# Performance work log

Hardware: AMD Instinct MI355X
Metric: run time of the kernel (lower is better)

The kernel has to match this reference:

```python
import jax, jax.numpy as jnp
import numpy as np
from functools import partial

BANK = 256
ADDR = 64
OUT_C, IN_C, KH, KW = 64, 64, 3, 3
BS, H, W = 32, 128, 128


def setup_inputs() -> dict:
    key = jax.random.key(0)
    ks = jax.random.split(key, 6)
    x = jax.random.normal(ks[0], (BS, IN_C, H, W), dtype=jnp.float32)
    w_addr = jax.random.normal(ks[1], (BS, ADDR), dtype=jnp.float32)
    b_addr = jax.random.normal(ks[2], (BS, OUT_C, ADDR), dtype=jnp.float32)
    # learned parameters
    w_bank = jax.random.normal(ks[3], (BANK, OUT_C, IN_C, KH, KW), dtype=jnp.float32) * (1.0 / np.sqrt(IN_C * KH * KW))
    bound = 1.0 / np.sqrt(IN_C * KH * KW)
    b_bank = jax.random.uniform(ks[4], (BANK,), minval=-bound, maxval=bound, dtype=jnp.float32)
    address_space = jax.random.normal(ks[5], (BANK, ADDR), dtype=jnp.float32)
    return {"x": x, "w_addr": w_addr, "b_addr": b_addr, "w_bank": w_bank,
            "b_bank": b_bank, "address_space": address_space, "s": 1, "p": 1}


def _hyper_conv(x, w_addr, b_addr, w_bank, b_bank, address_space, s, p):
    # soft addressing: keys @ address_space.T -> softmax -> weighted sum of bank
    sel_w = jax.nn.softmax(w_addr @ address_space.T, axis=-1)          # [bs, bank]
    w = jnp.einsum('bn,noikl->boikl', sel_w, w_bank)                   # [bs, O, I, kh, kw]
    sel_b = jax.nn.softmax(b_addr @ address_space.T, axis=-1)          # [bs, O, bank]
    b = jnp.einsum('bon,n->bo', sel_b, b_bank)                         # [bs, O]

    def conv_one(xi, wi):
        # xi: [I, H, W], wi: [O, I, kh, kw]
        return jax.lax.conv_general_dilated(
            xi[None], wi, window_strides=(s, s), padding=[(p, p), (p, p)],
            dimension_numbers=('NCHW', 'OIHW', 'NCHW'))[0]

    o = jax.vmap(conv_one)(x, w)                                       # [bs, O, H', W']
    return o + b[:, :, None, None]


def reference(x, w_addr, b_addr, w_bank, b_bank, address_space, s, p):
    return _hyper_conv(x, w_addr, b_addr, w_bank, b_bank, address_space, int(s), int(p))
```

## Files before the change

### kernel.cpp

```cpp
#include <hip/hip_runtime.h>
#include <hip/hip_bf16.h>
#include <math.h>

#define BS   32
#define IC   64
#define OC   64
#define HH   128
#define WW   128
#define BANK 256
#define ADDR 64
#define WELEM (OC*IC*9)

#define XROW  (8 * 132 * 8)
#define XSAMP (130 * XROW)

typedef short short8 __attribute__((ext_vector_type(8)));
typedef float f32x16 __attribute__((ext_vector_type(16)));

__device__ __forceinline__ short f2bf(float f) {
    unsigned u = __builtin_bit_cast(unsigned, f);
    unsigned r = (u + 0x7FFFu + ((u >> 16) & 1u)) >> 16;
    return (short)r;
}

typedef __attribute__((address_space(3))) unsigned int lds_u32;
typedef const __attribute__((address_space(1))) unsigned int g_u32;
__device__ __forceinline__ void gload16(const short* g, short* l) {
    __builtin_amdgcn_global_load_lds((g_u32*)g, (lds_u32*)l, 16, 0, 0);
}

__global__ __launch_bounds__(BANK) void k_selw(const float* __restrict__ w_addr,
                                               const float* __restrict__ aspace,
                                               float* __restrict__ sel_w) {
    int b = blockIdx.x;
    int n = threadIdx.x;
    const float* wa = w_addr + b * ADDR;
    const float* as = aspace + n * ADDR;
    float dot = 0.f;
#pragma unroll
    for (int k = 0; k < ADDR; ++k) dot = fmaf(wa[k], as[k], dot);

    __shared__ float red[BANK];
    red[n] = dot; __syncthreads();
    for (int s = BANK / 2; s > 0; s >>= 1) {
        if (n < s) red[n] = fmaxf(red[n], red[n + s]);
        __syncthreads();
    }
    float m = red[0]; __syncthreads();
    float e = expf(dot - m);
    red[n] = e; __syncthreads();
    for (int s = BANK / 2; s > 0; s >>= 1) {
        if (n < s) red[n] += red[n + s];
        __syncthreads();
    }
    sel_w[b * BANK + n] = e / red[0];
}

__global__ __launch_bounds__(BANK) void k_bias(const float* __restrict__ b_addr,
                                               const float* __restrict__ aspace,
                                               const float* __restrict__ b_bank,
                                               float* __restrict__ bias) {
    int bo = blockIdx.x;
    int n  = threadIdx.x;
    const float* ba = b_addr + (size_t)bo * ADDR;
    const float* as = aspace + n * ADDR;
    float dot = 0.f;
#pragma unroll
    for (int k = 0; k < ADDR; ++k) dot = fmaf(ba[k], as[k], dot);

    __shared__ float red[BANK];
    red[n] = dot; __syncthreads();
    for (int s = BANK / 2; s > 0; s >>= 1) {
        if (n < s) red[n] = fmaxf(red[n], red[n + s]);
        __syncthreads();
    }
    float m = red[0]; __syncthreads();
    float e = expf(dot - m);
    red[n] = e; __syncthreads();
    for (int s = BANK / 2; s > 0; s >>= 1) {
        if (n < s) red[n] += red[n + s];
        __syncthreads();
    }
    float denom = red[0]; __syncthreads();
    red[n] = e * b_bank[n]; __syncthreads();
    for (int s = BANK / 2; s > 0; s >>= 1) {
        if (n < s) red[n] += red[n + s];
        __syncthreads();
    }
    if (n == 0) bias[bo] = red[0] / denom;
}

__global__ __launch_bounds__(256) void k_wmix(const float* __restrict__ sel_w,
                                              const float* __restrict__ w_bank,
                                              __hip_bfloat16* __restrict__ wmb) {
    __shared__ float s_red[4 * 32 * 64];

    int tid = threadIdx.x;
    int jl  = tid & 63;
    int c   = tid >> 6;
    int jb  = blockIdx.x * 64 + jl;

    int n0 = __builtin_amdgcn_readfirstlane(c * 64);
    const float* selp = sel_w + n0;

    float wv[64];
#pragma unroll
    for (int n = 0; n < 64; ++n)
        wv[n] = w_bank[(size_t)(n0 + n) * WELEM + jb];

    float acc[BS];
#pragma unroll
    for (int b = 0; b < BS; ++b) acc[b] = 0.f;
#pragma unroll
    for (int b = 0; b < BS; ++b)
#pragma unroll
        for (int n = 0; n < 64; ++n)
            acc[b] = fmaf(selp[b * BANK + n], wv[n], acc[b]);

#pragma unroll
    for (int b = 0; b < BS; ++b)
        s_red[(c * 32 + b) * 64 + jl] = acc[b];
    __syncthreads();

    int B0  = (tid * 8) & 31;
    int jl2 = (tid * 8) >> 5;
    int j   = blockIdx.x * 64 + jl2;
    int o   = j / 576;
    int rem = j - o * 576;
    int i   = rem / 9;
    int tap = rem - i * 9;
    size_t base = ((size_t)tap * 8 + (i >> 3)) * 512 + (size_t)o * 8 + (i & 7);
#pragma unroll
    for (int u = 0; u < 8; ++u) {
        int b = B0 + u;
        float v = s_red[(0 * 32 + b) * 64 + jl2] + s_red[(1 * 32 + b) * 64 + jl2]
                + s_red[(2 * 32 + b) * 64 + jl2] + s_red[(3 * 32 + b) * 64 + jl2];
        short sv = f2bf(v);
        wmb[(size_t)b * (9 * 8 * 64 * 8) + base] = *reinterpret_cast<__hip_bfloat16*>(&sv);
    }
}

__global__ __launch_bounds__(256) void k_tr(const float* __restrict__ x,
                                            short* __restrict__ xbf) {
    int bid = blockIdx.x;
    int b  = bid / 130;
    int ry = bid - b * 130;
    short* row = xbf + (size_t)b * XSAMP + (size_t)ry * XROW;
    int tid = threadIdx.x;
    short8 z = {0, 0, 0, 0, 0, 0, 0, 0};

    if (ry == 0 || ry == 129) {
        for (int u = tid; u < 1056; u += 256)
            *(short8*)(row + u * 8) = z;
        return;
    }
    int gy = ry - 1;
    const float* xb = x + ((size_t)b * IC * HH + gy) * WW;
    int icg = tid & 7;
    int px0 = (tid >> 3) * 4;

    float4 v[8];
#pragma unroll
    for (int e = 0; e < 8; ++e)
        v[e] = *(const float4*)&xb[(size_t)(icg * 8 + e) * HH * WW + px0];
#pragma unroll
    for (int p = 0; p < 4; ++p) {
        short8 s;
#pragma unroll
        for (int e = 0; e < 8; ++e)
            s[e] = f2bf(((const float*)&v[e])[p]);
        *(short8*)(row + ((size_t)icg * 132 + px0 + p + 1) * 8) = s;
    }
    if (tid < 32) {
        int g = tid >> 2;
        int sel = tid & 3;
        int cz = (sel == 0) ? 0 : (128 + sel);
        *(short8*)(row + ((size_t)g * 132 + cz) * 8) = z;
    }
}

__global__ __launch_bounds__(512) void k_conv(const short* __restrict__ xbf,
                                              const short* __restrict__ wmb,
                                              const float* __restrict__ bias,
                                              float* __restrict__ out) {
    __shared__ short s_x[2][8704];
    __shared__ short s_w[2][9216];
    __shared__ float s_bias[OC];

    int orig    = blockIdx.x;
    int logical = (orig & 7) * 256 + (orig >> 3);
    int b   = logical >> 6;
    int y0  = (logical & 63) * 2;
    int tid = threadIdx.x;
    int wv  = tid >> 6;
    int lane = tid & 63;
    int h   = lane >> 5;
    int ln  = lane & 31;
    int wr  = wv & 1;
    int oh  = (wv >> 1) & 1;
    int ph  = wv >> 2;

    if (tid < OC) s_bias[tid] = bias[b * OC + tid];

    const short* xs   = xbf + (size_t)b * XSAMP + (size_t)y0 * XROW;
    const short* wmbs = wmb + (size_t)b * 36864;

    auto stage = [&](int cc, int bf) {
        for (int i = wv; i < 17; i += 8) {
            int u  = i * 64 + lane;
            int uc = (u < 1056) ? u : 0;
            int ky  = uc / 264;
            int rem = uc - ky * 264;
            const short* g = xs + (size_t)ky * XROW + (size_t)(2 * cc * 132 + rem) * 8;
            gload16(g, &s_x[bf][i * 512]);
        }
        for (int j = wv; j < 18; j += 8) {
            int v   = j * 64 + lane;
            int tap = v >> 7;
            int wt  = v & 127;
            const short* g = wmbs + (size_t)((tap * 8 + 2 * cc) * 64 + wt) * 8;
            gload16(g, &s_w[bf][j * 512]);
        }
    };

    f32x16 acc[2];
    acc[0] = (f32x16)0.0f;
    acc[1] = (f32x16)0.0f;

    stage(0, 0);
    __syncthreads();

    for (int cc = 0; cc < 4; ++cc) {
        int bf = cc & 1;
        if (cc < 3) stage(cc + 1, bf ^ 1);
        const short8* xb8 = (const short8*)s_x[bf];
        const short8* wb8 = (const short8*)s_w[bf];
#pragma unroll
        for (int ky = 0; ky < 3; ++ky) {
#pragma unroll
            for (int kx = 0; kx < 3; ++kx) {
                short8 a = wb8[((ky * 3 + kx) * 2 + h) * 64 + oh * 32 + ln];
#pragma unroll
                for (int nt = 0; nt < 2; ++nt) {
                    short8 bb = xb8[((wr + ky) * 2 + h) * 132 + ph * 64 + nt * 32 + ln + kx];
                    acc[nt] = __builtin_amdgcn_mfma_f32_32x32x16_bf16(a, bb, acc[nt], 0, 0, 0);
                }
            }
        }
        __syncthreads();
    }

    int y = y0 + wr;
    float* ob = out + (size_t)b * OC * HH * WW;
#pragma unroll
    for (int nt = 0; nt < 2; ++nt) {
#pragma unroll
        for (int r = 0; r < 16; ++r) {
            int oc = oh * 32 + (r & 3) + 8 * (r >> 2) + 4 * h;
            int px = ph * 64 + nt * 32 + ln;
            ob[((size_t)oc * HH + y) * WW + px] = acc[nt][r] + s_bias[oc];
        }
    }
}

extern "C" void kernel_launch(void* const* d_in, const int* in_sizes, int n_in,
                              void* d_out, int out_size, void* d_ws, size_t ws_size,
                              hipStream_t stream) {
    const float* x      = (const float*)d_in[0];
    const float* w_addr = (const float*)d_in[1];
    const float* b_addr = (const float*)d_in[2];
    const float* w_bank = (const float*)d_in[3];
    const float* b_bank = (const float*)d_in[4];
    const float* aspace = (const float*)d_in[5];
    float* out = (float*)d_out;

    char* ws = (char*)d_ws;
    float*          sel_w = (float*)ws;
    float*          bias  = (float*)(ws + 32768);
    __hip_bfloat16* wmb   = (__hip_bfloat16*)(ws + 40960);
    short*          xbf   = (short*)(ws + 40960 + 2359296);

    k_selw<<<BS, BANK, 0, stream>>>(w_addr, aspace, sel_w);
    k_bias<<<BS * OC, BANK, 0, stream>>>(b_addr, aspace, b_bank, bias);
    k_wmix<<<WELEM / 64, 256, 0, stream>>>(sel_w, w_bank, wmb);
    k_tr<<<BS * 130, 256, 0, stream>>>(x, xbf);
    k_conv<<<BS * 64, 512, 0, stream>>>(xbf, (const short*)wmb, bias, out);
}
```

Before: 156.0 us.

## Fuse fp32-to-bf16 input transpose into conv kernel with register-staged prefetch

Removes the separate k_tr kernel and its padded bf16 scratch copy of x. The conv kernel now reads fp32 x directly, converts and packs it to bf16 on the fly, and writes it into LDS along with zeroed halo columns and zero rows at the borders. Loads for the next channel chunk go into registers before the MFMA loop and are stored to LDS after it, replacing the async global_load_lds copies. This saves one full read and write of x plus a launch. In exchange it adds register pressure (launch_bounds 512,4), conversion work inside the conv, and redundant reads of x rows across neighbouring row blocks.

```diff
diff --git a/kernel.cpp b/kernel.cpp
--- a/kernel.cpp
+++ b/kernel.cpp
@@ -10,9 +10,7 @@
 #define BANK 256
 #define ADDR 64
 #define WELEM (OC*IC*9)
-
-#define XROW  (8 * 132 * 8)
-#define XSAMP (130 * XROW)
+#define PLANE (HH*WW)
 
 typedef short short8 __attribute__((ext_vector_type(8)));
 typedef float f32x16 __attribute__((ext_vector_type(16)));
@@ -23,10 +21,12 @@
     return (short)r;
 }
 
-typedef __attribute__((address_space(3))) unsigned int lds_u32;
-typedef const __attribute__((address_space(1))) unsigned int g_u32;
-__device__ __forceinline__ void gload16(const short* g, short* l) {
-    __builtin_amdgcn_global_load_lds((g_u32*)g, (lds_u32*)l, 16, 0, 0);
+__device__ __forceinline__ unsigned pack_bf2(float lo, float hi) {
+    unsigned ul = __builtin_bit_cast(unsigned, lo);
+    unsigned uh = __builtin_bit_cast(unsigned, hi);
+    unsigned rl = (ul + 0x7FFFu + ((ul >> 16) & 1u)) >> 16;
+    unsigned rh = (uh + 0x7FFFu + ((uh >> 16) & 1u)) & 0xFFFF0000u;
+    return rh | (rl & 0xFFFFu);
 }
 
 __global__ __launch_bounds__(BANK) void k_selw(const float* __restrict__ w_addr,
@@ -140,99 +140,112 @@
     }
 }
 
-__global__ __launch_bounds__(256) void k_tr(const float* __restrict__ x,
-                                            short* __restrict__ xbf) {
-    int bid = blockIdx.x;
-    int b  = bid / 130;
-    int ry = bid - b * 130;
-    short* row = xbf + (size_t)b * XSAMP + (size_t)ry * XROW;
-    int tid = threadIdx.x;
-    short8 z = {0, 0, 0, 0, 0, 0, 0, 0};
-
-    if (ry == 0 || ry == 129) {
-        for (int u = tid; u < 1056; u += 256)
-            *(short8*)(row + u * 8) = z;
-        return;
-    }
-    int gy = ry - 1;
-    const float* xb = x + ((size_t)b * IC * HH + gy) * WW;
-    int icg = tid & 7;
-    int px0 = (tid >> 3) * 4;
-
-    float4 v[8];
-#pragma unroll
-    for (int e = 0; e < 8; ++e)
-        v[e] = *(const float4*)&xb[(size_t)(icg * 8 + e) * HH * WW + px0];
-#pragma unroll
-    for (int p = 0; p < 4; ++p) {
-        short8 s;
-#pragma unroll
-        for (int e = 0; e < 8; ++e)
-            s[e] = f2bf(((const float*)&v[e])[p]);
-        *(short8*)(row + ((size_t)icg * 132 + px0 + p + 1) * 8) = s;
-    }
-    if (tid < 32) {
-        int g = tid >> 2;
-        int sel = tid & 3;
-        int cz = (sel == 0) ? 0 : (128 + sel);
-        *(short8*)(row + ((size_t)g * 132 + cz) * 8) = z;
-    }
-}
-
-__global__ __launch_bounds__(512) void k_conv(const short* __restrict__ xbf,
-                                              const short* __restrict__ wmb,
-                                              const float* __restrict__ bias,
-                                              float* __restrict__ out) {
-    __shared__ short s_x[2][8704];
-    __shared__ short s_w[2][9216];
+__global__ __launch_bounds__(512, 4) void k_conv(const float* __restrict__ x,
+                                                 const short* __restrict__ wmb,
+                                                 const float* __restrict__ bias,
+                                                 float* __restrict__ out) {
+    __shared__ short s_x[2][4 * 2 * 132 * 8];
+    __shared__ short s_w[2][9 * 2 * 64 * 8];
     __shared__ float s_bias[OC];
 
     int orig    = blockIdx.x;
     int logical = (orig & 7) * 256 + (orig >> 3);
-    int b   = logical >> 6;
-    int y0  = (logical & 63) * 2;
-    int tid = threadIdx.x;
-    int wv  = tid >> 6;
+    int b    = logical >> 6;
+    int y0   = (logical & 63) * 2;
+    int tid  = threadIdx.x;
     int lane = tid & 63;
-    int h   = lane >> 5;
-    int ln  = lane & 31;
-    int wr  = wv & 1;
-    int oh  = (wv >> 1) & 1;
-    int ph  = wv >> 2;
+    int wv   = tid >> 6;
+    int h    = lane >> 5;
+    int ln   = lane & 31;
+    int wr   = wv & 1;
+    int oh   = (wv >> 1) & 1;
+    int ph   = wv >> 2;
 
     if (tid < OC) s_bias[tid] = bias[b * OC + tid];
-
-    const short* xs   = xbf + (size_t)b * XSAMP + (size_t)y0 * XROW;
+    if (tid < 32) {
+        int bf   = tid >> 4;
+        int kg   = (tid >> 1) & 7;
+        int col  = (tid & 1) ? 129 : 0;
+        *(short8*)&s_x[bf][(kg * 132 + col) * 8] = (short8){0,0,0,0,0,0,0,0};
+    }
+
+    const float* xb   = x + (size_t)b * IC * PLANE;
     const short* wmbs = wmb + (size_t)b * 36864;
 
-    auto stage = [&](int cc, int bf) {
-        for (int i = wv; i < 17; i += 8) {
-            int u  = i * 64 + lane;
-            int uc = (u < 1056) ? u : 0;
-            int ky  = uc / 264;
-            int rem = uc - ky * 264;
-            const short* g = xs + (size_t)ky * XROW + (size_t)(2 * cc * 132 + rem) * 8;
-            gload16(g, &s_x[bf][i * 512]);
+    int x_ky[2], x_icp[2], x_colq[2]; bool x_ok[2];
+#pragma unroll
+    for (int k = 0; k < 2; ++k) {
+        int u = k * 512 + tid;
+        x_colq[k] = u & 31;
+        x_icp[k]  = (u >> 5) & 7;
+        x_ky[k]   = u >> 8;
+        int gy = y0 - 1 + x_ky[k];
+        x_ok[k] = ((unsigned)gy < (unsigned)HH);
+    }
+    bool w_val[3]; int w_tap[3], w_g[3], w_oc[3];
+#pragma unroll
+    for (int k = 0; k < 3; ++k) {
+        int v = k * 512 + tid;
+        w_val[k] = (v < 1152);
+        int vv = w_val[k] ? v : 0;
+        w_tap[k] = vv >> 7; w_g[k] = (vv >> 6) & 1; w_oc[k] = vv & 63;
+    }
+
+    float4 xlo[2], xhi[2];
+    short8 wreg[3];
+
+    auto LOAD = [&](int cc) {
+#pragma unroll
+        for (int k = 0; k < 2; ++k) {
+            if (x_ok[k]) {
+                const float* p = xb + (size_t)(cc * 16 + 2 * x_icp[k]) * PLANE
+                               + (y0 - 1 + x_ky[k]) * WW + x_colq[k] * 4;
+                xlo[k] = *(const float4*)p;
+                xhi[k] = *(const float4*)(p + PLANE);
+            } else {
+                xlo[k] = make_float4(0.f, 0.f, 0.f, 0.f);
+                xhi[k] = make_float4(0.f, 0.f, 0.f, 0.f);
+            }
         }
-        for (int j = wv; j < 18; j += 8) {
-            int v   = j * 64 + lane;
-            int tap = v >> 7;
-            int wt  = v & 127;
-            const short* g = wmbs + (size_t)((tap * 8 + 2 * cc) * 64 + wt) * 8;
-            gload16(g, &s_w[bf][j * 512]);
+#pragma unroll
+        for (int k = 0; k < 3; ++k)
+            if (w_val[k])
+                wreg[k] = *(const short8*)(wmbs +
+                    (size_t)((w_tap[k] * 8 + 2 * cc + w_g[k]) * 64 + w_oc[k]) * 8);
+    };
+    auto STORE = [&](int bf) {
+        unsigned* sx32 = (unsigned*)s_x[bf];
+#pragma unroll
+        for (int k = 0; k < 2; ++k) {
+            int g  = x_icp[k] >> 2;
+            int pi = x_icp[k] & 3;
+            int rowbase = (x_ky[k] * 2 + g) * 132;
+#pragma unroll
+            for (int j = 0; j < 4; ++j) {
+                unsigned pk = pack_bf2(((const float*)&xlo[k])[j],
+                                       ((const float*)&xhi[k])[j]);
+                int col = x_colq[k] * 4 + 1 + j;
+                sx32[((rowbase + col) * 8 + pi * 2) >> 1] = pk;
+            }
         }
+#pragma unroll
+        for (int k = 0; k < 3; ++k)
+            if (w_val[k])
+                *(short8*)&s_w[bf][((w_tap[k] * 2 + w_g[k]) * 64 + w_oc[k]) * 8] = wreg[k];
     };
 
     f32x16 acc[2];
     acc[0] = (f32x16)0.0f;
     acc[1] = (f32x16)0.0f;
 
-    stage(0, 0);
+    LOAD(0);
+    STORE(0);
     __syncthreads();
 
+#pragma unroll
     for (int cc = 0; cc < 4; ++cc) {
         int bf = cc & 1;
-        if (cc < 3) stage(cc + 1, bf ^ 1);
+        if (cc < 3) LOAD(cc + 1);
         const short8* xb8 = (const short8*)s_x[bf];
         const short8* wb8 = (const short8*)s_w[bf];
 #pragma unroll
@@ -247,11 +260,12 @@
                 }
             }
         }
+        if (cc < 3) STORE(bf ^ 1);
         __syncthreads();
     }
 
     int y = y0 + wr;
-    float* ob = out + (size_t)b * OC * HH * WW;
+    float* ob = out + (size_t)b * OC * PLANE;
 #pragma unroll
     for (int nt = 0; nt < 2; ++nt) {
 #pragma unroll
@@ -278,11 +292,9 @@
     float*          sel_w = (float*)ws;
     float*          bias  = (float*)(ws + 32768);
     __hip_bfloat16* wmb   = (__hip_bfloat16*)(ws + 40960);
-    short*          xbf   = (short*)(ws + 40960 + 2359296);
 
     k_selw<<<BS, BANK, 0, stream>>>(w_addr, aspace, sel_w);
     k_bias<<<BS * OC, BANK, 0, stream>>>(b_addr, aspace, b_bank, bias);
     k_wmix<<<WELEM / 64, 256, 0, stream>>>(sel_w, w_bank, wmb);
-    k_tr<<<BS * 130, 256, 0, stream>>>(x, xbf);
-    k_conv<<<BS * 64, 512, 0, stream>>>(xbf, (const short*)wmb, bias, out);
-}
+    k_conv<<<BS * 64, 512, 0, stream>>>(x, (const short*)wmb, bias, out);
+}
```

New measurement: 137.3 us. 1.14x faster.

## Load conv weights directly to registers and simplify input staging

Applied to the files above, without the earlier changes.

The conv kernel stops staging mixed weights through LDS: each wave now loads its nine A-fragments straight from global memory into registers every channel chunk, which halves the shared-memory footprint. Input staging is rewritten so each wave copies one contiguous row segment, and the launch bounds now request higher occupancy. The weight-mix kernel streams bank weights in chunks of eight instead of holding 64 values in registers, cutting register pressure. The trade-off is that global weight loads now sit directly in the MFMA loop and are repeated by every wave, so their latency is no longer hidden behind the LDS double buffer.

```diff
diff --git a/kernel.cpp b/kernel.cpp
--- a/kernel.cpp
+++ b/kernel.cpp
@@ -10,6 +10,7 @@
 #define BANK 256
 #define ADDR 64
 #define WELEM (OC*IC*9)
+#define PLANE (HH*WW)
 
 #define XROW  (8 * 132 * 8)
 #define XSAMP (130 * XROW)
@@ -103,19 +104,21 @@
     int n0 = __builtin_amdgcn_readfirstlane(c * 64);
     const float* selp = sel_w + n0;
 
-    float wv[64];
-#pragma unroll
-    for (int n = 0; n < 64; ++n)
-        wv[n] = w_bank[(size_t)(n0 + n) * WELEM + jb];
-
     float acc[BS];
 #pragma unroll
     for (int b = 0; b < BS; ++b) acc[b] = 0.f;
-#pragma unroll
-    for (int b = 0; b < BS; ++b)
-#pragma unroll
-        for (int n = 0; n < 64; ++n)
-            acc[b] = fmaf(selp[b * BANK + n], wv[n], acc[b]);
+
+    for (int nb = 0; nb < 8; ++nb) {
+        float wv[8];
+#pragma unroll
+        for (int i = 0; i < 8; ++i)
+            wv[i] = w_bank[(size_t)(n0 + nb * 8 + i) * WELEM + jb];
+#pragma unroll
+        for (int b = 0; b < BS; ++b)
+#pragma unroll
+            for (int i = 0; i < 8; ++i)
+                acc[b] = fmaf(selp[b * BANK + nb * 8 + i], wv[i], acc[b]);
+    }
 
 #pragma unroll
     for (int b = 0; b < BS; ++b)
@@ -179,67 +182,63 @@
     }
 }
 
-__global__ __launch_bounds__(512) void k_conv(const short* __restrict__ xbf,
-                                              const short* __restrict__ wmb,
-                                              const float* __restrict__ bias,
-                                              float* __restrict__ out) {
-    __shared__ short s_x[2][8704];
-    __shared__ short s_w[2][9216];
+__global__ __launch_bounds__(512, 8) void k_conv(const short* __restrict__ xbf,
+                                                 const short* __restrict__ wmb,
+                                                 const float* __restrict__ bias,
+                                                 float* __restrict__ out) {
+    __shared__ short s_x[2][1056 * 8];
     __shared__ float s_bias[OC];
 
     int orig    = blockIdx.x;
     int logical = (orig & 7) * 256 + (orig >> 3);
-    int b   = logical >> 6;
-    int y0  = (logical & 63) * 2;
-    int tid = threadIdx.x;
-    int wv  = tid >> 6;
+    int b    = logical >> 6;
+    int y0   = (logical & 63) * 2;
+    int tid  = threadIdx.x;
     int lane = tid & 63;
-    int h   = lane >> 5;
-    int ln  = lane & 31;
-    int wr  = wv & 1;
-    int oh  = (wv >> 1) & 1;
-    int ph  = wv >> 2;
+    int wv   = tid >> 6;
+    int h    = lane >> 5;
+    int ln   = lane & 31;
+    int wr   = wv & 1;
+    int oh   = (wv >> 1) & 1;
+    int ph   = wv >> 2;
 
     if (tid < OC) s_bias[tid] = bias[b * OC + tid];
 
     const short* xs   = xbf + (size_t)b * XSAMP + (size_t)y0 * XROW;
     const short* wmbs = wmb + (size_t)b * 36864;
 
-    auto stage = [&](int cc, int bf) {
-        for (int i = wv; i < 17; i += 8) {
-            int u  = i * 64 + lane;
-            int uc = (u < 1056) ? u : 0;
-            int ky  = uc / 264;
-            int rem = uc - ky * 264;
-            const short* g = xs + (size_t)ky * XROW + (size_t)(2 * cc * 132 + rem) * 8;
-            gload16(g, &s_x[bf][i * 512]);
-        }
-        for (int j = wv; j < 18; j += 8) {
-            int v   = j * 64 + lane;
-            int tap = v >> 7;
-            int wt  = v & 127;
-            const short* g = wmbs + (size_t)((tap * 8 + 2 * cc) * 64 + wt) * 8;
-            gload16(g, &s_w[bf][j * 512]);
-        }
+    int sky = wv >> 1, sgg = wv & 1;
+    auto STAGEX = [&](int cc, int bf) {
+        const short* gb = xs + (size_t)sky * XROW + (size_t)(2 * cc + sgg) * 1056;
+        short* lb = &s_x[bf][(sky * 2 + sgg) * 132 * 8];
+        gload16(gb + (size_t)lane * 8, lb);
+        gload16(gb + (size_t)(64 + lane) * 8, lb + 64 * 8);
+        if (lane < 4) gload16(gb + (size_t)(128 + lane) * 8, lb + 128 * 8);
     };
 
     f32x16 acc[2];
     acc[0] = (f32x16)0.0f;
     acc[1] = (f32x16)0.0f;
 
-    stage(0, 0);
+    STAGEX(0, 0);
     __syncthreads();
 
     for (int cc = 0; cc < 4; ++cc) {
         int bf = cc & 1;
-        if (cc < 3) stage(cc + 1, bf ^ 1);
+        if (cc < 3) STAGEX(cc + 1, bf ^ 1);
+
+        short8 areg[9];
+#pragma unroll
+        for (int tap = 0; tap < 9; ++tap)
+            areg[tap] = *(const short8*)(wmbs +
+                (size_t)((tap * 8 + 2 * cc + h) * 64 + oh * 32 + ln) * 8);
+
         const short8* xb8 = (const short8*)s_x[bf];
-        const short8* wb8 = (const short8*)s_w[bf];
 #pragma unroll
         for (int ky = 0; ky < 3; ++ky) {
 #pragma unroll
             for (int kx = 0; kx < 3; ++kx) {
-                short8 a = wb8[((ky * 3 + kx) * 2 + h) * 64 + oh * 32 + ln];
+                short8 a = areg[ky * 3 + kx];
 #pragma unroll
                 for (int nt = 0; nt < 2; ++nt) {
                     short8 bb = xb8[((wr + ky) * 2 + h) * 132 + ph * 64 + nt * 32 + ln + kx];
@@ -251,7 +250,7 @@
     }
 
     int y = y0 + wr;
-    float* ob = out + (size_t)b * OC * HH * WW;
+    float* ob = out + (size_t)b * OC * PLANE;
 #pragma unroll
     for (int nt = 0; nt < 2; ++nt) {
 #pragma unroll
```

Result: slower. 165.0 us (+5.8%).
